# Kernel optimization log

Hardware: AMD Instinct MI355X
Metric: run time of the kernel (lower is better)

The kernel has to match this reference:

```python
import jax, jax.numpy as jnp
import numpy as np

HID, VOCAB, LAYERS, MAXLEN, SPAN = 1024, 32000, 4, 128, 2


def setup_inputs() -> dict:
    key = jax.random.key(0)
    ks = jax.random.split(key, 12)
    s = 0.02
    return {
        "input_ids": jax.random.randint(ks[0], (SPAN,), 0, VOCAB),
        "hidden": jax.random.normal(ks[1], (LAYERS, 1, HID), jnp.float32),
        "encoder_outputs": jax.random.normal(ks[2], (MAXLEN, HID), jnp.float32),
        "embedding": jax.random.normal(ks[3], (VOCAB, HID), jnp.float32) * s,
        "attn_W": jax.random.normal(ks[4], (MAXLEN, HID * (1 + SPAN)), jnp.float32) * s,
        "attn_b": jnp.zeros((MAXLEN,), jnp.float32),
        "comb_W": jax.random.normal(ks[5], (HID, HID * (1 + SPAN)), jnp.float32) * s,
        "comb_b": jnp.zeros((HID,), jnp.float32),
        "gru_Wih": jax.random.normal(ks[6], (LAYERS, 3 * HID, HID), jnp.float32) * s,
        "gru_Whh": jax.random.normal(ks[7], (LAYERS, 3 * HID, HID), jnp.float32) * s,
        "gru_bih": jnp.zeros((LAYERS, 3 * HID), jnp.float32),
        "gru_bhh": jnp.zeros((LAYERS, 3 * HID), jnp.float32),
        "out_W": jax.random.normal(ks[8], (VOCAB * SPAN, HID), jnp.float32) * s,
        "out_b": jnp.zeros((VOCAB * SPAN,), jnp.float32),
    }


def reference(input_ids, hidden, encoder_outputs, embedding, attn_W, attn_b,
              comb_W, comb_b, gru_Wih, gru_Whh, gru_bih, gru_bhh, out_W, out_b):
    # embed span tokens -> [1, SPAN*HID] (dropout = identity at eval)
    emb = embedding[input_ids].reshape(1, SPAN * HID)
    # attention over encoder outputs
    attn_in = jnp.concatenate([emb, hidden[0]], axis=1)          # [1, (1+SPAN)*HID]
    attn_weights = jax.nn.softmax(attn_in @ attn_W.T + attn_b, axis=1)  # [1, MAXLEN]
    attn_applied = attn_weights @ encoder_outputs                 # [1, HID]
    # combine + relu -> GRU input
    x = jax.nn.relu(jnp.concatenate([emb, attn_applied], axis=1) @ comb_W.T + comb_b)  # [1, HID]
    # multi-layer GRU single step (PyTorch gate order: r, z, n)
    new_h = []
    inp = x
    for l in range(LAYERS):
        h = hidden[l]                                             # [1, HID]
        gi = inp @ gru_Wih[l].T + gru_bih[l]                      # [1, 3*HID]
        gh = h @ gru_Whh[l].T + gru_bhh[l]
        i_r, i_z, i_n = jnp.split(gi, 3, axis=1)
        h_r, h_z, h_n = jnp.split(gh, 3, axis=1)
        r = jax.nn.sigmoid(i_r + h_r)
        z = jax.nn.sigmoid(i_z + h_z)
        n = jnp.tanh(i_n + r * h_n)
        h2 = (1.0 - z) * n + z * h
        new_h.append(h2)
        inp = h2
    hidden_new = jnp.stack(new_h)                                 # [LAYERS, 1, HID]
    # output projection, split into SPAN vocab chunks, log_softmax each
    logits = inp @ out_W.T + out_b                                # [1, SPAN*VOCAB]
    logp = jax.nn.log_softmax(logits.reshape(SPAN, VOCAB), axis=-1)  # [SPAN, VOCAB]
    return logp, hidden_new, attn_weights
```

## Files before the change

kernel.cpp:

```cpp
#include <hip/hip_runtime.h>
#include <math.h>

#define HID 1024
#define VOCAB 32000
#define LAYERS 4
#define MAXLEN 128
#define SPAN 2

#define OUT_LOGP 0
#define OUT_HID 64000
#define OUT_ATTNW 68096

#define WS_XCAT 0
#define WS_SCORES 3072
#define WS_X 3200
#define WS_RED 4224
#define WS_LOGITS 8192

__global__ __launch_bounds__(256) void k_scores(const int* __restrict__ ids,
                                                const float* __restrict__ hidden,
                                                const float* __restrict__ embedding,
                                                const float* __restrict__ attn_W,
                                                const float* __restrict__ attn_b,
                                                float* __restrict__ ws) {
    int b = blockIdx.x;
    int t = threadIdx.x;
    if (b < MAXLEN) {
        const float4* W4 = (const float4*)(attn_W + (size_t)b * 3072);
        float sum = 0.f;
#pragma unroll
        for (int i = 0; i < 3; i++) {
            int k4 = t + 256 * i;
            float4 w = W4[k4];
            int e = k4 * 4;
            float4 x;
            if (e < 2048) {
                int row = ids[e >> 10];
                x = *(const float4*)(embedding + (size_t)row * HID + (e & 1023));
            } else {
                x = *(const float4*)(hidden + (e - 2048));
            }
            sum += w.x * x.x + w.y * x.y + w.z * x.z + w.w * x.w;
        }
        __shared__ float sred[4];
        int lane = t & 63, wid = t >> 6;
        for (int o = 32; o > 0; o >>= 1) sum += __shfl_down(sum, o, 64);
        if (lane == 0) sred[wid] = sum;
        __syncthreads();
        if (t == 0) {
            float v = sred[0] + sred[1] + sred[2] + sred[3];
            ws[WS_SCORES + b] = v + attn_b[b];
        }
    } else {
        int idx = (b - MAXLEN) * 256 + t;
        int row = ids[idx >> 10];
        ws[WS_XCAT + idx] = embedding[(size_t)row * HID + (idx & 1023)];
    }
}

__global__ __launch_bounds__(128) void k_softmax_apply(const float* __restrict__ enc,
                                                       float* __restrict__ ws,
                                                       float* __restrict__ out) {
    __shared__ float w[MAXLEN];
    __shared__ float red[2];
    int t = threadIdx.x;
    int lane = t & 63, wid = t >> 6;
    float s = ws[WS_SCORES + t];
    float m = s;
    for (int o = 32; o > 0; o >>= 1) m = fmaxf(m, __shfl_down(m, o, 64));
    if (lane == 0) red[wid] = m;
    __syncthreads();
    float gmax = fmaxf(red[0], red[1]);
    __syncthreads();
    float e = expf(s - gmax);
    float sum = e;
    for (int o = 32; o > 0; o >>= 1) sum += __shfl_down(sum, o, 64);
    if (lane == 0) red[wid] = sum;
    __syncthreads();
    float gsum = red[0] + red[1];
    float wt = e / gsum;
    w[t] = wt;
    if (blockIdx.x == 0) out[OUT_ATTNW + t] = wt;
    __syncthreads();
    int i = blockIdx.x * 128 + t;
    float acc = 0.f;
#pragma unroll 8
    for (int k = 0; k < MAXLEN; k++) acc += w[k] * enc[(size_t)k * HID + i];
    ws[WS_XCAT + 2048 + i] = acc;
}

__global__ __launch_bounds__(256) void k_comb(const float* __restrict__ comb_W,
                                              const float* __restrict__ comb_b,
                                              float* __restrict__ ws) {
    int r = blockIdx.x, t = threadIdx.x;
    const float4* W4 = (const float4*)(comb_W + (size_t)r * 3072);
    const float4* x4 = (const float4*)(ws + WS_XCAT);
    float sum = 0.f;
#pragma unroll
    for (int i = 0; i < 3; i++) {
        int k4 = t + 256 * i;
        float4 w = W4[k4];
        float4 x = x4[k4];
        sum += w.x * x.x + w.y * x.y + w.z * x.z + w.w * x.w;
    }
    __shared__ float sred[4];
    int lane = t & 63, wid = t >> 6;
    for (int o = 32; o > 0; o >>= 1) sum += __shfl_down(sum, o, 64);
    if (lane == 0) sred[wid] = sum;
    __syncthreads();
    if (t == 0) {
        float v = sred[0] + sred[1] + sred[2] + sred[3];
        ws[WS_X + r] = fmaxf(v + comb_b[r], 0.f);
    }
}

__global__ __launch_bounds__(384) void k_gru(const float* __restrict__ inp,
                                             const float* __restrict__ h,
                                             const float* __restrict__ Wih,
                                             const float* __restrict__ Whh,
                                             const float* __restrict__ bih,
                                             const float* __restrict__ bhh,
                                             float* __restrict__ h_out) {
    int j = blockIdx.x;
    int t = threadIdx.x;
    int wv = t >> 6, lane = t & 63;
    __shared__ float dots[6];
    const float* W;
    const float* x;
    if (wv < 3) { W = Wih + ((size_t)wv * HID + j) * HID; x = inp; }
    else        { W = Whh + ((size_t)(wv - 3) * HID + j) * HID; x = h; }
    const float4* W4 = (const float4*)W;
    const float4* x4 = (const float4*)x;
    float sum = 0.f;
#pragma unroll
    for (int i = 0; i < 4; i++) {
        float4 w = W4[lane + 64 * i];
        float4 xx = x4[lane + 64 * i];
        sum += w.x * xx.x + w.y * xx.y + w.z * xx.z + w.w * xx.w;
    }
    for (int o = 32; o > 0; o >>= 1) sum += __shfl_down(sum, o, 64);
    if (lane == 0) dots[wv] = sum;
    __syncthreads();
    if (t == 0) {
        float ir = dots[0] + bih[j];
        float iz = dots[1] + bih[HID + j];
        float in_ = dots[2] + bih[2 * HID + j];
        float hr = dots[3] + bhh[j];
        float hz = dots[4] + bhh[HID + j];
        float hn = dots[5] + bhh[2 * HID + j];
        float rg = 1.f / (1.f + expf(-(ir + hr)));
        float zg = 1.f / (1.f + expf(-(iz + hz)));
        float ng = tanhf(in_ + rg * hn);
        h_out[j] = (1.f - zg) * ng + zg * h[j];
    }
}

__global__ __launch_bounds__(256) void k_logits(const float* __restrict__ h3,
                                                const float* __restrict__ out_W,
                                                const float* __restrict__ out_b,
                                                float* __restrict__ ws) {
    int wv = threadIdx.x >> 6, lane = threadIdx.x & 63;
    int row = blockIdx.x * 4 + wv;
    const float4* W4 = (const float4*)(out_W + (size_t)row * HID);
    const float4* x4 = (const float4*)h3;
    float sum = 0.f;
#pragma unroll
    for (int i = 0; i < 4; i++) {
        float4 w = W4[lane + 64 * i];
        float4 x = x4[lane + 64 * i];
        sum += w.x * x.x + w.y * x.y + w.z * x.z + w.w * x.w;
    }
    for (int o = 32; o > 0; o >>= 1) sum += __shfl_down(sum, o, 64);
    if (lane == 0) ws[WS_LOGITS + row] = sum + out_b[row];
}

__global__ __launch_bounds__(1024) void k_red(float* __restrict__ ws) {
    int s = blockIdx.x, t = threadIdx.x;
    int lane = t & 63, wid = t >> 6;
    const float* l = ws + WS_LOGITS + (size_t)s * VOCAB;
    __shared__ float sred[16];
    __shared__ float bcast;
    float m = -INFINITY;
    for (int i = t; i < VOCAB; i += 1024) m = fmaxf(m, l[i]);
    for (int o = 32; o > 0; o >>= 1) m = fmaxf(m, __shfl_down(m, o, 64));
    if (lane == 0) sred[wid] = m;
    __syncthreads();
    if (t == 0) {
        float v = -INFINITY;
        for (int k = 0; k < 16; k++) v = fmaxf(v, sred[k]);
        bcast = v;
    }
    __syncthreads();
    float gmax = bcast;
    __syncthreads();
    float sum = 0.f;
    for (int i = t; i < VOCAB; i += 1024) sum += expf(l[i] - gmax);
    for (int o = 32; o > 0; o >>= 1) sum += __shfl_down(sum, o, 64);
    if (lane == 0) sred[wid] = sum;
    __syncthreads();
    if (t == 0) {
        float v = 0.f;
        for (int k = 0; k < 16; k++) v += sred[k];
        ws[WS_RED + s] = gmax;
        ws[WS_RED + 2 + s] = logf(v);
    }
}

__global__ __launch_bounds__(256) void k_logp(const float* __restrict__ ws,
                                              float* __restrict__ out) {
    int i = blockIdx.x * 256 + threadIdx.x;
    if (i < SPAN * VOCAB) {
        int s = i / VOCAB;
        out[OUT_LOGP + i] = ws[WS_LOGITS + i] - ws[WS_RED + s] - ws[WS_RED + 2 + s];
    }
}

extern "C" void kernel_launch(void* const* d_in, const int* in_sizes, int n_in,
                              void* d_out, int out_size, void* d_ws, size_t ws_size,
                              hipStream_t stream) {
    const int* ids = (const int*)d_in[0];
    const float* hidden = (const float*)d_in[1];
    const float* enc = (const float*)d_in[2];
    const float* embedding = (const float*)d_in[3];
    const float* attn_W = (const float*)d_in[4];
    const float* attn_b = (const float*)d_in[5];
    const float* comb_W = (const float*)d_in[6];
    const float* comb_b = (const float*)d_in[7];
    const float* gru_Wih = (const float*)d_in[8];
    const float* gru_Whh = (const float*)d_in[9];
    const float* gru_bih = (const float*)d_in[10];
    const float* gru_bhh = (const float*)d_in[11];
    const float* out_W = (const float*)d_in[12];
    const float* out_b = (const float*)d_in[13];
    float* out = (float*)d_out;
    float* ws = (float*)d_ws;

    k_scores<<<136, 256, 0, stream>>>(ids, hidden, embedding, attn_W, attn_b, ws);
    k_softmax_apply<<<8, 128, 0, stream>>>(enc, ws, out);
    k_comb<<<1024, 256, 0, stream>>>(comb_W, comb_b, ws);
    for (int l = 0; l < LAYERS; l++) {
        const float* inp = (l == 0) ? (ws + WS_X) : (out + OUT_HID + (l - 1) * HID);
        k_gru<<<1024, 384, 0, stream>>>(inp,
                                        hidden + (size_t)l * HID,
                                        gru_Wih + (size_t)l * 3 * HID * HID,
                                        gru_Whh + (size_t)l * 3 * HID * HID,
                                        gru_bih + (size_t)l * 3 * HID,
                                        gru_bhh + (size_t)l * 3 * HID,
                                        out + OUT_HID + l * HID);
    }
    k_logits<<<16000, 256, 0, stream>>>(out + OUT_HID + 3 * HID, out_W, out_b, ws);
    k_red<<<2, 1024, 0, stream>>>(ws);
    k_logp<<<250, 256, 0, stream>>>(ws, out);
}
```

Baseline: 517.4 us.

## Compute four logit rows per wave and split log-softmax reduction across 64 blocks

```diff
diff --git a/kernel.cpp b/kernel.cpp
--- a/kernel.cpp
+++ b/kernel.cpp
@@ -84,7 +84,7 @@
     __syncthreads();
     int i = blockIdx.x * 128 + t;
     float acc = 0.f;
-#pragma unroll 8
+#pragma unroll 16
     for (int k = 0; k < MAXLEN; k++) acc += w[k] * enc[(size_t)k * HID + i];
     ws[WS_XCAT + 2048 + i] = acc;
 }
@@ -160,59 +160,76 @@
                                                 const float* __restrict__ out_b,
                                                 float* __restrict__ ws) {
     int wv = threadIdx.x >> 6, lane = threadIdx.x & 63;
-    int row = blockIdx.x * 4 + wv;
-    const float4* W4 = (const float4*)(out_W + (size_t)row * HID);
+    int r0 = (blockIdx.x * 4 + wv) * 4;
     const float4* x4 = (const float4*)h3;
-    float sum = 0.f;
-#pragma unroll
-    for (int i = 0; i < 4; i++) {
-        float4 w = W4[lane + 64 * i];
-        float4 x = x4[lane + 64 * i];
-        sum += w.x * x.x + w.y * x.y + w.z * x.z + w.w * x.w;
-    }
-    for (int o = 32; o > 0; o >>= 1) sum += __shfl_down(sum, o, 64);
-    if (lane == 0) ws[WS_LOGITS + row] = sum + out_b[row];
-}
-
-__global__ __launch_bounds__(1024) void k_red(float* __restrict__ ws) {
-    int s = blockIdx.x, t = threadIdx.x;
+    float4 xv[4];
+#pragma unroll
+    for (int i = 0; i < 4; i++) xv[i] = x4[lane + 64 * i];
+    const float4* W4 = (const float4*)(out_W + (size_t)r0 * HID);
+    float s[4] = {0.f, 0.f, 0.f, 0.f};
+#pragma unroll
+    for (int r = 0; r < 4; r++) {
+#pragma unroll
+        for (int i = 0; i < 4; i++) {
+            float4 w = W4[r * 256 + lane + 64 * i];
+            s[r] += w.x * xv[i].x + w.y * xv[i].y + w.z * xv[i].z + w.w * xv[i].w;
+        }
+    }
+#pragma unroll
+    for (int r = 0; r < 4; r++)
+        for (int o = 32; o > 0; o >>= 1) s[r] += __shfl_down(s[r], o, 64);
+    if (lane == 0) {
+        float4 b = *(const float4*)(out_b + r0);
+        float4 res = make_float4(s[0] + b.x, s[1] + b.y, s[2] + b.z, s[3] + b.w);
+        *(float4*)(ws + WS_LOGITS + r0) = res;
+    }
+}
+
+__global__ __launch_bounds__(256) void k_red(float* __restrict__ ws) {
+    int b = blockIdx.x, t = threadIdx.x;
+    int span = b >> 5, chunk = b & 31;
     int lane = t & 63, wid = t >> 6;
-    const float* l = ws + WS_LOGITS + (size_t)s * VOCAB;
-    __shared__ float sred[16];
-    __shared__ float bcast;
+    const float* l = ws + WS_LOGITS + (size_t)span * VOCAB + chunk * 1000;
+    __shared__ float sred[4];
     float m = -INFINITY;
-    for (int i = t; i < VOCAB; i += 1024) m = fmaxf(m, l[i]);
+    for (int i = t; i < 1000; i += 256) m = fmaxf(m, l[i]);
     for (int o = 32; o > 0; o >>= 1) m = fmaxf(m, __shfl_down(m, o, 64));
     if (lane == 0) sred[wid] = m;
     __syncthreads();
+    float gmax = fmaxf(fmaxf(sred[0], sred[1]), fmaxf(sred[2], sred[3]));
+    __syncthreads();
+    float sum = 0.f;
+    for (int i = t; i < 1000; i += 256) sum += expf(l[i] - gmax);
+    for (int o = 32; o > 0; o >>= 1) sum += __shfl_down(sum, o, 64);
+    if (lane == 0) sred[wid] = sum;
+    __syncthreads();
     if (t == 0) {
-        float v = -INFINITY;
-        for (int k = 0; k < 16; k++) v = fmaxf(v, sred[k]);
-        bcast = v;
-    }
-    __syncthreads();
-    float gmax = bcast;
-    __syncthreads();
-    float sum = 0.f;
-    for (int i = t; i < VOCAB; i += 1024) sum += expf(l[i] - gmax);
-    for (int o = 32; o > 0; o >>= 1) sum += __shfl_down(sum, o, 64);
-    if (lane == 0) sred[wid] = sum;
-    __syncthreads();
-    if (t == 0) {
-        float v = 0.f;
-        for (int k = 0; k < 16; k++) v += sred[k];
-        ws[WS_RED + s] = gmax;
-        ws[WS_RED + 2 + s] = logf(v);
+        ws[WS_RED + b * 2] = gmax;
+        ws[WS_RED + b * 2 + 1] = sred[0] + sred[1] + sred[2] + sred[3];
     }
 }
 
 __global__ __launch_bounds__(256) void k_logp(const float* __restrict__ ws,
                                               float* __restrict__ out) {
-    int i = blockIdx.x * 256 + threadIdx.x;
-    if (i < SPAN * VOCAB) {
-        int s = i / VOCAB;
-        out[OUT_LOGP + i] = ws[WS_LOGITS + i] - ws[WS_RED + s] - ws[WS_RED + 2 + s];
-    }
+    int t = threadIdx.x;
+    int i = blockIdx.x * 256 + t;
+    int span = blockIdx.x / 125;
+    __shared__ float gm_s, ls_s;
+    if (t < 64) {
+        float m = -INFINITY, sm = 0.f;
+        if (t < 32) {
+            m = ws[WS_RED + (span * 32 + t) * 2];
+            sm = ws[WS_RED + (span * 32 + t) * 2 + 1];
+        }
+        float gm = m;
+        for (int o = 32; o > 0; o >>= 1) gm = fmaxf(gm, __shfl_down(gm, o, 64));
+        gm = __shfl(gm, 0, 64);
+        float e = sm * expf(m - gm);
+        for (int o = 32; o > 0; o >>= 1) e += __shfl_down(e, o, 64);
+        if (t == 0) { gm_s = gm; ls_s = logf(e); }
+    }
+    __syncthreads();
+    out[OUT_LOGP + i] = ws[WS_LOGITS + i] - gm_s - ls_s;
 }
 
 extern "C" void kernel_launch(void* const* d_in, const int* in_sizes, int n_in,
@@ -248,7 +265,7 @@
                                         gru_bhh + (size_t)l * 3 * HID,
                                         out + OUT_HID + l * HID);
     }
-    k_logits<<<16000, 256, 0, stream>>>(out + OUT_HID + 3 * HID, out_W, out_b, ws);
-    k_red<<<2, 1024, 0, stream>>>(ws);
+    k_logits<<<4000, 256, 0, stream>>>(out + OUT_HID + 3 * HID, out_W, out_b, ws);
+    k_red<<<64, 256, 0, stream>>>(ws);
     k_logp<<<250, 256, 0, stream>>>(ws, out);
 }
```

New measurement: 513.4 us. About the same (-0.8%).

## Fuse whole decoder step into one cooperative persistent kernel with grid syncs

Applied to the files above, without the earlier changes.

```diff
diff --git a/kernel.cpp b/kernel.cpp
--- a/kernel.cpp
+++ b/kernel.cpp
@@ -1,5 +1,8 @@
 #include <hip/hip_runtime.h>
+#include <hip/hip_cooperative_groups.h>
 #include <math.h>
+
+namespace cg = cooperative_groups;
 
 #define HID 1024
 #define VOCAB 32000
@@ -14,204 +17,258 @@
 #define WS_XCAT 0
 #define WS_SCORES 3072
 #define WS_X 3200
-#define WS_RED 4224
+#define WS_RED 4352
 #define WS_LOGITS 8192
 
-__global__ __launch_bounds__(256) void k_scores(const int* __restrict__ ids,
-                                                const float* __restrict__ hidden,
-                                                const float* __restrict__ embedding,
-                                                const float* __restrict__ attn_W,
-                                                const float* __restrict__ attn_b,
-                                                float* __restrict__ ws) {
-    int b = blockIdx.x;
-    int t = threadIdx.x;
-    if (b < MAXLEN) {
-        const float4* W4 = (const float4*)(attn_W + (size_t)b * 3072);
+__device__ __forceinline__ float dot4(float4 a, float4 b) {
+    return a.x * b.x + a.y * b.y + a.z * b.z + a.w * b.w;
+}
+
+__global__ __launch_bounds__(1024, 4) void mega(
+    const int* __restrict__ ids,
+    const float* __restrict__ hidden,
+    const float* __restrict__ enc,
+    const float* __restrict__ embedding,
+    const float* __restrict__ attn_W,
+    const float* __restrict__ attn_b,
+    const float* __restrict__ comb_W,
+    const float* __restrict__ comb_b,
+    const float* __restrict__ gru_Wih,
+    const float* __restrict__ gru_Whh,
+    const float* __restrict__ gru_bih,
+    const float* __restrict__ gru_bhh,
+    const float* __restrict__ out_W,
+    const float* __restrict__ out_b,
+    float* __restrict__ out,
+    float* __restrict__ ws)
+{
+    cg::grid_group grid = cg::this_grid();
+    const int b = blockIdx.x;
+    const int t = threadIdx.x;
+    const int wv = t >> 6;
+    const int lane = t & 63;
+
+    __shared__ float sred[16];
+    __shared__ float ssum[16];
+    __shared__ float w2[MAXLEN];
+    __shared__ float part[8][MAXLEN];
+    __shared__ float gdots[24];
+
+    if (b < 32) {
+        int gw = b * 16 + wv;
+        int row = gw >> 2, q = gw & 3;
+        const float4* W4 = (const float4*)(attn_W + (size_t)row * 3072);
         float sum = 0.f;
 #pragma unroll
         for (int i = 0; i < 3; i++) {
-            int k4 = t + 256 * i;
+            int k4 = q * 192 + lane + 64 * i;
             float4 w = W4[k4];
             int e = k4 * 4;
             float4 x;
             if (e < 2048) {
-                int row = ids[e >> 10];
-                x = *(const float4*)(embedding + (size_t)row * HID + (e & 1023));
+                int r = ids[e >> 10];
+                x = *(const float4*)(embedding + (size_t)r * HID + (e & 1023));
             } else {
                 x = *(const float4*)(hidden + (e - 2048));
             }
-            sum += w.x * x.x + w.y * x.y + w.z * x.z + w.w * x.w;
-        }
-        __shared__ float sred[4];
-        int lane = t & 63, wid = t >> 6;
+            sum += dot4(w, x);
+        }
         for (int o = 32; o > 0; o >>= 1) sum += __shfl_down(sum, o, 64);
-        if (lane == 0) sred[wid] = sum;
+        if (lane == 0) sred[wv] = sum;
+        __syncthreads();
+        if (t < 4) {
+            int r = b * 4 + t;
+            ws[WS_SCORES + r] = sred[4 * t] + sred[4 * t + 1] + sred[4 * t + 2] + sred[4 * t + 3] + attn_b[r];
+        }
+    } else if (b < 34) {
+        int idx = (b - 32) * 1024 + t;
+        int r = ids[idx >> 10];
+        ws[WS_XCAT + idx] = embedding[(size_t)r * HID + (idx & 1023)];
+    }
+    grid.sync();
+
+    if (b < 8) {
+        if (t < 128) w2[t] = ws[WS_SCORES + t];
+        __syncthreads();
+        float m = -INFINITY;
+        for (int k = 0; k < 128; k++) m = fmaxf(m, w2[k]);
+        float s = 0.f;
+        for (int k = 0; k < 128; k++) s += expf(w2[k] - m);
+        __syncthreads();
+        if (t < 128) w2[t] = expf(w2[t] - m) / s;
+        __syncthreads();
+        int col = b * 128 + (t & 127);
+        int seg = t >> 7;
+        float p = 0.f;
+#pragma unroll
+        for (int k = 0; k < 16; k++)
+            p += w2[seg * 16 + k] * enc[(size_t)(seg * 16 + k) * HID + col];
+        part[seg][t & 127] = p;
+        __syncthreads();
+        if (t < 128) {
+            float acc = 0.f;
+#pragma unroll
+            for (int s2 = 0; s2 < 8; s2++) acc += part[s2][t];
+            ws[WS_XCAT + 2048 + col] = acc;
+            if (b == 0) out[OUT_ATTNW + t] = w2[t];
+        }
+    }
+    grid.sync();
+
+    {
+        int r0 = b * 4;
+        int row = r0 + (wv & 3), q = wv >> 2;
+        const float4* W4 = (const float4*)(comb_W + (size_t)row * 3072);
+        const float4* x4 = (const float4*)(ws + WS_XCAT);
+        float sum = 0.f;
+#pragma unroll
+        for (int i = 0; i < 3; i++) {
+            int k4 = q * 192 + lane + 64 * i;
+            sum += dot4(W4[k4], x4[k4]);
+        }
+        for (int o = 32; o > 0; o >>= 1) sum += __shfl_down(sum, o, 64);
+        if (lane == 0) sred[wv] = sum;
+        __syncthreads();
+        if (t < 4) {
+            float v = sred[t] + sred[t + 4] + sred[t + 8] + sred[t + 12] + comb_b[r0 + t];
+            ws[WS_X + r0 + t] = fmaxf(v, 0.f);
+        }
+    }
+    grid.sync();
+
+    for (int l = 0; l < LAYERS; l++) {
+        const float* inp = (l == 0) ? (ws + WS_X) : (out + OUT_HID + (l - 1) * HID);
+        const float* h = hidden + (size_t)l * HID;
+        const float* Wih = gru_Wih + (size_t)l * 3 * HID * HID;
+        const float* Whh = gru_Whh + (size_t)l * 3 * HID * HID;
+        const float* bih = gru_bih + (size_t)l * 3 * HID;
+        const float* bhh = gru_bhh + (size_t)l * 3 * HID;
+        int j0 = b * 4;
+        if (wv < 12) {
+            int da = 2 * wv, db = da + 1;
+            int jla = da & 3, ga = da >> 2;
+            int jlb = db & 3, gb = db >> 2;
+            const float* Wra = (ga < 3) ? (Wih + ((size_t)ga * HID + j0 + jla) * HID)
+                                        : (Whh + ((size_t)(ga - 3) * HID + j0 + jla) * HID);
+            const float* Wrb = (gb < 3) ? (Wih + ((size_t)gb * HID + j0 + jlb) * HID)
+                                        : (Whh + ((size_t)(gb - 3) * HID + j0 + jlb) * HID);
+            const float4* xa4 = (const float4*)((ga < 3) ? inp : h);
+            const float4* xb4 = (const float4*)((gb < 3) ? inp : h);
+            const float4* Wa4 = (const float4*)Wra;
+            const float4* Wb4 = (const float4*)Wrb;
+            float sa = 0.f, sb = 0.f;
+#pragma unroll
+            for (int i = 0; i < 4; i++) {
+                int k4 = lane + 64 * i;
+                sa += dot4(Wa4[k4], xa4[k4]);
+                sb += dot4(Wb4[k4], xb4[k4]);
+            }
+            for (int o = 32; o > 0; o >>= 1) {
+                sa += __shfl_down(sa, o, 64);
+                sb += __shfl_down(sb, o, 64);
+            }
+            if (lane == 0) { gdots[da] = sa; gdots[db] = sb; }
+        }
+        __syncthreads();
+        if (t < 4) {
+            int j = j0 + t;
+            float ir = gdots[0 * 4 + t] + bih[j];
+            float iz = gdots[1 * 4 + t] + bih[HID + j];
+            float in_ = gdots[2 * 4 + t] + bih[2 * HID + j];
+            float hr = gdots[3 * 4 + t] + bhh[j];
+            float hz = gdots[4 * 4 + t] + bhh[HID + j];
+            float hn = gdots[5 * 4 + t] + bhh[2 * HID + j];
+            float rg = 1.f / (1.f + expf(-(ir + hr)));
+            float zg = 1.f / (1.f + expf(-(iz + hz)));
+            float ng = tanhf(in_ + rg * hn);
+            out[OUT_HID + l * HID + j] = (1.f - zg) * ng + zg * h[j];
+        }
+        grid.sync();
+    }
+
+    {
+        int r0 = b * 250;
+        const float4* x4 = (const float4*)(out + OUT_HID + 3 * HID);
+        float4 xv[4];
+#pragma unroll
+        for (int i = 0; i < 4; i++) xv[i] = x4[lane + 64 * i];
+        float m = -INFINITY, s = 0.f;
+        for (int i = 0; i < 8; i++) {
+            int oa = wv + 32 * i;
+            int ob = oa + 16;
+            bool vb = (ob < 250);
+            int ra = r0 + oa;
+            int rb = r0 + (vb ? ob : 0);
+            const float4* Wa = (const float4*)(out_W + (size_t)ra * HID);
+            const float4* Wb = (const float4*)(out_W + (size_t)rb * HID);
+            float sa = 0.f, sb = 0.f;
+            if (vb) {
+#pragma unroll
+                for (int k = 0; k < 4; k++) {
+                    int k4 = lane + 64 * k;
+                    sa += dot4(Wa[k4], xv[k]);
+                    sb += dot4(Wb[k4], xv[k]);
+                }
+            } else {
+#pragma unroll
+                for (int k = 0; k < 4; k++) {
+                    int k4 = lane + 64 * k;
+                    sa += dot4(Wa[k4], xv[k]);
+                }
+            }
+            for (int o = 32; o > 0; o >>= 1) {
+                sa += __shfl_down(sa, o, 64);
+                sb += __shfl_down(sb, o, 64);
+            }
+            if (lane == 0) {
+                float v = sa + out_b[ra];
+                ws[WS_LOGITS + ra] = v;
+                if (v > m) { s = s * expf(m - v) + 1.f; m = v; } else { s += expf(v - m); }
+                if (vb) {
+                    float v2 = sb + out_b[rb];
+                    ws[WS_LOGITS + rb] = v2;
+                    if (v2 > m) { s = s * expf(m - v2) + 1.f; m = v2; } else { s += expf(v2 - m); }
+                }
+            }
+        }
+        if (lane == 0) { sred[wv] = m; ssum[wv] = s; }
         __syncthreads();
         if (t == 0) {
-            float v = sred[0] + sred[1] + sred[2] + sred[3];
-            ws[WS_SCORES + b] = v + attn_b[b];
-        }
-    } else {
-        int idx = (b - MAXLEN) * 256 + t;
-        int row = ids[idx >> 10];
-        ws[WS_XCAT + idx] = embedding[(size_t)row * HID + (idx & 1023)];
-    }
-}
-
-__global__ __launch_bounds__(128) void k_softmax_apply(const float* __restrict__ enc,
-                                                       float* __restrict__ ws,
-                                                       float* __restrict__ out) {
-    __shared__ float w[MAXLEN];
-    __shared__ float red[2];
-    int t = threadIdx.x;
-    int lane = t & 63, wid = t >> 6;
-    float s = ws[WS_SCORES + t];
-    float m = s;
-    for (int o = 32; o > 0; o >>= 1) m = fmaxf(m, __shfl_down(m, o, 64));
-    if (lane == 0) red[wid] = m;
-    __syncthreads();
-    float gmax = fmaxf(red[0], red[1]);
-    __syncthreads();
-    float e = expf(s - gmax);
-    float sum = e;
-    for (int o = 32; o > 0; o >>= 1) sum += __shfl_down(sum, o, 64);
-    if (lane == 0) red[wid] = sum;
-    __syncthreads();
-    float gsum = red[0] + red[1];
-    float wt = e / gsum;
-    w[t] = wt;
-    if (blockIdx.x == 0) out[OUT_ATTNW + t] = wt;
-    __syncthreads();
-    int i = blockIdx.x * 128 + t;
-    float acc = 0.f;
-#pragma unroll 8
-    for (int k = 0; k < MAXLEN; k++) acc += w[k] * enc[(size_t)k * HID + i];
-    ws[WS_XCAT + 2048 + i] = acc;
-}
-
-__global__ __launch_bounds__(256) void k_comb(const float* __restrict__ comb_W,
-                                              const float* __restrict__ comb_b,
-                                              float* __restrict__ ws) {
-    int r = blockIdx.x, t = threadIdx.x;
-    const float4* W4 = (const float4*)(comb_W + (size_t)r * 3072);
-    const float4* x4 = (const float4*)(ws + WS_XCAT);
-    float sum = 0.f;
-#pragma unroll
-    for (int i = 0; i < 3; i++) {
-        int k4 = t + 256 * i;
-        float4 w = W4[k4];
-        float4 x = x4[k4];
-        sum += w.x * x.x + w.y * x.y + w.z * x.z + w.w * x.w;
-    }
-    __shared__ float sred[4];
-    int lane = t & 63, wid = t >> 6;
-    for (int o = 32; o > 0; o >>= 1) sum += __shfl_down(sum, o, 64);
-    if (lane == 0) sred[wid] = sum;
-    __syncthreads();
-    if (t == 0) {
-        float v = sred[0] + sred[1] + sred[2] + sred[3];
-        ws[WS_X + r] = fmaxf(v + comb_b[r], 0.f);
-    }
-}
-
-__global__ __launch_bounds__(384) void k_gru(const float* __restrict__ inp,
-                                             const float* __restrict__ h,
-                                             const float* __restrict__ Wih,
-                                             const float* __restrict__ Whh,
-                                             const float* __restrict__ bih,
-                                             const float* __restrict__ bhh,
-                                             float* __restrict__ h_out) {
-    int j = blockIdx.x;
-    int t = threadIdx.x;
-    int wv = t >> 6, lane = t & 63;
-    __shared__ float dots[6];
-    const float* W;
-    const float* x;
-    if (wv < 3) { W = Wih + ((size_t)wv * HID + j) * HID; x = inp; }
-    else        { W = Whh + ((size_t)(wv - 3) * HID + j) * HID; x = h; }
-    const float4* W4 = (const float4*)W;
-    const float4* x4 = (const float4*)x;
-    float sum = 0.f;
-#pragma unroll
-    for (int i = 0; i < 4; i++) {
-        float4 w = W4[lane + 64 * i];
-        float4 xx = x4[lane + 64 * i];
-        sum += w.x * xx.x + w.y * xx.y + w.z * xx.z + w.w * xx.w;
-    }
-    for (int o = 32; o > 0; o >>= 1) sum += __shfl_down(sum, o, 64);
-    if (lane == 0) dots[wv] = sum;
-    __syncthreads();
-    if (t == 0) {
-        float ir = dots[0] + bih[j];
-        float iz = dots[1] + bih[HID + j];
-        float in_ = dots[2] + bih[2 * HID + j];
-        float hr = dots[3] + bhh[j];
-        float hz = dots[4] + bhh[HID + j];
-        float hn = dots[5] + bhh[2 * HID + j];
-        float rg = 1.f / (1.f + expf(-(ir + hr)));
-        float zg = 1.f / (1.f + expf(-(iz + hz)));
-        float ng = tanhf(in_ + rg * hn);
-        h_out[j] = (1.f - zg) * ng + zg * h[j];
-    }
-}
-
-__global__ __launch_bounds__(256) void k_logits(const float* __restrict__ h3,
-                                                const float* __restrict__ out_W,
-                                                const float* __restrict__ out_b,
-                                                float* __restrict__ ws) {
-    int wv = threadIdx.x >> 6, lane = threadIdx.x & 63;
-    int row = blockIdx.x * 4 + wv;
-    const float4* W4 = (const float4*)(out_W + (size_t)row * HID);
-    const float4* x4 = (const float4*)h3;
-    float sum = 0.f;
-#pragma unroll
-    for (int i = 0; i < 4; i++) {
-        float4 w = W4[lane + 64 * i];
-        float4 x = x4[lane + 64 * i];
-        sum += w.x * x.x + w.y * x.y + w.z * x.z + w.w * x.w;
-    }
-    for (int o = 32; o > 0; o >>= 1) sum += __shfl_down(sum, o, 64);
-    if (lane == 0) ws[WS_LOGITS + row] = sum + out_b[row];
-}
-
-__global__ __launch_bounds__(1024) void k_red(float* __restrict__ ws) {
-    int s = blockIdx.x, t = threadIdx.x;
-    int lane = t & 63, wid = t >> 6;
-    const float* l = ws + WS_LOGITS + (size_t)s * VOCAB;
-    __shared__ float sred[16];
-    __shared__ float bcast;
-    float m = -INFINITY;
-    for (int i = t; i < VOCAB; i += 1024) m = fmaxf(m, l[i]);
-    for (int o = 32; o > 0; o >>= 1) m = fmaxf(m, __shfl_down(m, o, 64));
-    if (lane == 0) sred[wid] = m;
-    __syncthreads();
-    if (t == 0) {
-        float v = -INFINITY;
-        for (int k = 0; k < 16; k++) v = fmaxf(v, sred[k]);
-        bcast = v;
-    }
-    __syncthreads();
-    float gmax = bcast;
-    __syncthreads();
-    float sum = 0.f;
-    for (int i = t; i < VOCAB; i += 1024) sum += expf(l[i] - gmax);
-    for (int o = 32; o > 0; o >>= 1) sum += __shfl_down(sum, o, 64);
-    if (lane == 0) sred[wid] = sum;
-    __syncthreads();
-    if (t == 0) {
-        float v = 0.f;
-        for (int k = 0; k < 16; k++) v += sred[k];
-        ws[WS_RED + s] = gmax;
-        ws[WS_RED + 2 + s] = logf(v);
-    }
-}
-
-__global__ __launch_bounds__(256) void k_logp(const float* __restrict__ ws,
-                                              float* __restrict__ out) {
-    int i = blockIdx.x * 256 + threadIdx.x;
-    if (i < SPAN * VOCAB) {
-        int s = i / VOCAB;
-        out[OUT_LOGP + i] = ws[WS_LOGITS + i] - ws[WS_RED + s] - ws[WS_RED + 2 + s];
+            float M = -INFINITY, S = 0.f;
+            for (int k = 0; k < 16; k++) {
+                float mk = sred[k], sk = ssum[k];
+                if (mk > M) { S = S * expf(M - mk) + sk; M = mk; }
+                else S += sk * expf(mk - M);
+            }
+            ws[WS_RED + b * 2] = M;
+            ws[WS_RED + b * 2 + 1] = S;
+        }
+    }
+    grid.sync();
+
+    {
+        int span = b >> 7;
+        float M = -INFINITY, S = 0.f;
+        if (wv < 2) {
+            M = ws[WS_RED + span * 256 + t * 2];
+            S = ws[WS_RED + span * 256 + t * 2 + 1];
+            for (int o = 32; o > 0; o >>= 1) {
+                float Mo = __shfl_down(M, o, 64);
+                float So = __shfl_down(S, o, 64);
+                float nM = fmaxf(M, Mo);
+                S = S * expf(M - nM) + So * expf(Mo - nM);
+                M = nM;
+            }
+            if (lane == 0) { sred[wv] = M; ssum[wv] = S; }
+        }
+        __syncthreads();
+        float M0 = sred[0], S0 = ssum[0], M1 = sred[1], S1 = ssum[1];
+        float gm = fmaxf(M0, M1);
+        float lse = logf(S0 * expf(M0 - gm) + S1 * expf(M1 - gm));
+        if (t < 250) {
+            int i = b * 250 + t;
+            out[OUT_LOGP + i] = ws[WS_LOGITS + i] - gm - lse;
+        }
     }
 }
 
@@ -235,20 +292,11 @@
     float* out = (float*)d_out;
     float* ws = (float*)d_ws;
 
-    k_scores<<<136, 256, 0, stream>>>(ids, hidden, embedding, attn_W, attn_b, ws);
-    k_softmax_apply<<<8, 128, 0, stream>>>(enc, ws, out);
-    k_comb<<<1024, 256, 0, stream>>>(comb_W, comb_b, ws);
-    for (int l = 0; l < LAYERS; l++) {
-        const float* inp = (l == 0) ? (ws + WS_X) : (out + OUT_HID + (l - 1) * HID);
-        k_gru<<<1024, 384, 0, stream>>>(inp,
-                                        hidden + (size_t)l * HID,
-                                        gru_Wih + (size_t)l * 3 * HID * HID,
-                                        gru_Whh + (size_t)l * 3 * HID * HID,
-                                        gru_bih + (size_t)l * 3 * HID,
-                                        gru_bhh + (size_t)l * 3 * HID,
-                                        out + OUT_HID + l * HID);
-    }
-    k_logits<<<16000, 256, 0, stream>>>(out + OUT_HID + 3 * HID, out_W, out_b, ws);
-    k_red<<<2, 1024, 0, stream>>>(ws);
-    k_logp<<<250, 256, 0, stream>>>(ws, out);
+    void* kargs[] = {
+        (void*)&ids, (void*)&hidden, (void*)&enc, (void*)&embedding,
+        (void*)&attn_W, (void*)&attn_b, (void*)&comb_W, (void*)&comb_b,
+        (void*)&gru_Wih, (void*)&gru_Whh, (void*)&gru_bih, (void*)&gru_bhh,
+        (void*)&out_W, (void*)&out_b, (void*)&out, (void*)&ws
+    };
+    hipLaunchCooperativeKernel((void*)mega, dim3(256), dim3(1024), kargs, 0, stream);
 }
```

After: 734.9 us. +42.0%, slower.
